# Kernel optimization log

Hardware: AMD Instinct MI355X
Metric: run time of the kernel (lower is better)

The kernel has to match this reference:

```python
import jax, jax.numpy as jnp
import numpy as np
from jax import lax

C = 128; NH = 8; DH = 16      # attn_channels, heads, head_dim
DI = 256; DS = 16; DC = 4     # hmb d_inner=expand*C, d_state, d_conv
KTOP = 128                    # max(min_focus_tokens, int(W*0.5))
CR = 64; CI = 128             # radar / image channels


def _ln(x, g, b, eps=1e-5):
    m = jnp.mean(x, -1, keepdims=True)
    v = jnp.mean((x - m) ** 2, -1, keepdims=True)
    return (x - m) * lax.rsqrt(v + eps) * g + b


def _conv1x1(x, w):
    return jnp.einsum('bchw,oc->bohw', x, w)


def _forward(image_features, radar_features, W_img, W_rad, g_q, b_q, g_kv, b_kv, g2, b2,
             Ws1, bs1, Ws2, bs2, Wqkv, bqkv, Wo, bo, Wf1, bf1, Wf2, bf2, W_delta,
             gamma, gamma_hmb, Wg, bg, Wfuse, bn_g, bn_b, bn_m, bn_v,
             W_hin, conv_dw, b_dw, W_dt, b_dt, W_Bp, W_Cp, A_log, Dp, W_hout):
    B, Cr, H, W = radar_features.shape
    N = B * H
    img_attn = _conv1x1(image_features, W_img)          # [B,C,H,W]
    rad_attn = _conv1x1(radar_features, W_rad)
    img_seq = img_attn.transpose(0, 2, 3, 1).reshape(N, W, C)
    rad_seq = rad_attn.transpose(0, 2, 3, 1).reshape(N, W, C)
    # progressive focus: per-row top-K image tokens
    si = jnp.concatenate([lax.stop_gradient(rad_seq), img_seq], -1)
    h1 = jax.nn.relu(si @ Ws1.T + bs1)
    score = (h1 @ Ws2.T + bs2)[..., 0]                  # [N,W]
    _, idx = lax.top_k(score, KTOP)
    img_kv = jnp.take_along_axis(img_seq, idx[:, :, None], axis=1)  # [N,K,C]
    # cross attention (torch MultiheadAttention, batch_first)
    q = _ln(rad_seq, g_q, b_q)
    kv = _ln(img_kv, g_kv, b_kv)
    Wq, Wk, Wv = Wqkv[:C], Wqkv[C:2 * C], Wqkv[2 * C:]
    bq_, bk_, bv_ = bqkv[:C], bqkv[C:2 * C], bqkv[2 * C:]
    qh = (q @ Wq.T + bq_).reshape(N, W, NH, DH)
    kh = (kv @ Wk.T + bk_).reshape(N, KTOP, NH, DH)
    vh = (kv @ Wv.T + bv_).reshape(N, KTOP, NH, DH)
    att = jax.nn.softmax(jnp.einsum('nqhd,nkhd->nhqk', qh, kh) / (DH ** 0.5), -1)
    ao = jnp.einsum('nhqk,nkhd->nqhd', att, vh).reshape(N, W, C) @ Wo.T + bo
    rad_seq = rad_seq + ao
    rad_seq = rad_seq + (jax.nn.relu(_ln(rad_seq, g2, b2) @ Wf1.T + bf1) @ Wf2.T + bf2)
    rad_bev = rad_seq.reshape(B, H, W, C).transpose(0, 3, 1, 2)
    delta_attn = _conv1x1(rad_bev, W_delta)
    # HMB-lite: bidirectional selective scan along x (per row)
    xz = _conv1x1(jnp.concatenate([rad_bev, img_attn], 1), W_hin)  # [B,2*DI,H,W]
    x, z = xz[:, :DI], xz[:, DI:]
    xr = x.transpose(0, 2, 1, 3).reshape(N, DI, W)
    zr = z.transpose(0, 2, 3, 1).reshape(N, W, DI)
    xp = jnp.pad(xr, ((0, 0), (0, 0), (DC - 1, 0)))     # causal depthwise conv
    xc = lax.conv_general_dilated(xp, conv_dw[:, None, :], (1,), 'VALID',
                                  feature_group_count=DI,
                                  dimension_numbers=('NCH', 'OIH', 'NCH'))
    xs = jax.nn.silu(xc + b_dw[:, None]).transpose(0, 2, 1)        # [N,W,DI]
    dt = jax.nn.softplus(xs @ W_dt.T + b_dt)            # [N,W,DI]
    Bt = xs @ W_Bp.T                                    # [N,W,DS]
    Ct = xs @ W_Cp.T
    A = -jnp.exp(A_log)                                 # [DI,DS]

    def scan(reverse):
        def step(h, inp):
            x_t, dt_t, B_t, C_t = inp
            h = jnp.exp(dt_t[..., None] * A) * h + (dt_t * x_t)[..., None] * B_t[:, None, :]
            return h, jnp.sum(h * C_t[:, None, :], -1)
        h0 = jnp.zeros((N, DI, DS), xs.dtype)
        seq = (xs.transpose(1, 0, 2), dt.transpose(1, 0, 2),
               Bt.transpose(1, 0, 2), Ct.transpose(1, 0, 2))
        _, ys = lax.scan(step, h0, seq, reverse=reverse)
        return ys.transpose(1, 0, 2)

    y = scan(False) + scan(True) + Dp * xs
    y = y * jax.nn.silu(zr)
    hmb = (y @ W_hout.T).reshape(B, H, W, C).transpose(0, 3, 1, 2)
    delta_hmb = _conv1x1(hmb, W_delta)
    # gate + range mask
    gate = jax.nn.sigmoid(_conv1x1(jnp.concatenate([radar_features, image_features], 1), Wg)
                          + bg[None, :, None, None])
    yv = jnp.arange(H, dtype=radar_features.dtype)
    wmask = jnp.clip(1.0 - 0.7 * yv / (H - 1), 0.3, None)
    gate = gate * wmask[None, None, :, None]
    radar_enh = radar_features + gamma * gate * delta_attn + gamma_hmb * gate * delta_hmb
    fuse_in = jnp.concatenate([radar_enh, image_features], 1)
    fo = lax.conv_general_dilated(fuse_in, Wfuse, (1, 1), 'SAME',
                                  dimension_numbers=('NCHW', 'OIHW', 'NCHW'))
    fo = ((fo - bn_m[None, :, None, None]) * lax.rsqrt(bn_v + 1e-5)[None, :, None, None]
          * bn_g[None, :, None, None] + bn_b[None, :, None, None])
    return jax.nn.relu(fo)


def setup_inputs():
    key = jax.random.key(0)
    ks = list(jax.random.split(key, 24))
    def rn(i, shape, s=0.05):
        return jax.random.normal(ks[i], shape, dtype=jnp.float32) * s
    B, H, W = 2, 256, 256
    return dict(
        image_features=jax.random.normal(ks[0], (B, CI, H, W), jnp.float32),
        radar_features=jax.random.normal(ks[1], (B, CR, H, W), jnp.float32),
        W_img=rn(2, (C, CI)), W_rad=rn(3, (C, CR)),
        g_q=jnp.ones(C), b_q=jnp.zeros(C), g_kv=jnp.ones(C), b_kv=jnp.zeros(C),
        g2=jnp.ones(C), b2=jnp.zeros(C),
        Ws1=rn(4, (64, 2 * C)), bs1=jnp.zeros(64), Ws2=rn(5, (1, 64)), bs2=jnp.zeros(1),
        Wqkv=rn(6, (3 * C, C)), bqkv=jnp.zeros(3 * C), Wo=rn(7, (C, C)), bo=jnp.zeros(C),
        Wf1=rn(8, (4 * C, C)), bf1=jnp.zeros(4 * C), Wf2=rn(9, (C, 4 * C)), bf2=jnp.zeros(C),
        W_delta=rn(10, (CR, C)),
        gamma=jnp.array(0.1, jnp.float32), gamma_hmb=jnp.array(0.05, jnp.float32),
        Wg=rn(11, (CR, CR + CI)), bg=jnp.zeros(CR),
        Wfuse=rn(12, (CR + CI, CR + CI, 3, 3)),
        bn_g=jnp.ones(CR + CI), bn_b=jnp.zeros(CR + CI),
        bn_m=jnp.zeros(CR + CI), bn_v=jnp.ones(CR + CI),
        W_hin=rn(13, (2 * DI, 2 * C)), conv_dw=rn(14, (DI, DC)), b_dw=jnp.zeros(DI),
        W_dt=rn(15, (DI, DI)), b_dt=jnp.full((DI,), 0.5, jnp.float32),
        W_Bp=rn(16, (DS, DI)), W_Cp=rn(17, (DS, DI)),
        A_log=jnp.log(jnp.broadcast_to(jnp.arange(1, DS + 1, dtype=jnp.float32), (DI, DS))),
        Dp=jnp.full((DI,), 0.01, jnp.float32),
        W_hout=rn(18, (C, DI)),
    )


def reference(image_features, radar_features, W_img, W_rad, g_q, b_q, g_kv, b_kv, g2, b2,
              Ws1, bs1, Ws2, bs2, Wqkv, bqkv, Wo, bo, Wf1, bf1, Wf2, bf2, W_delta,
              gamma, gamma_hmb, Wg, bg, Wfuse, bn_g, bn_b, bn_m, bn_v,
              W_hin, conv_dw, b_dw, W_dt, b_dt, W_Bp, W_Cp, A_log, Dp, W_hout):
    return _forward(image_features, radar_features, W_img, W_rad, g_q, b_q, g_kv, b_kv, g2, b2,
                    Ws1, bs1, Ws2, bs2, Wqkv, bqkv, Wo, bo, Wf1, bf1, Wf2, bf2, W_delta,
                    gamma, gamma_hmb, Wg, bg, Wfuse, bn_g, bn_b, bn_m, bn_v,
                    W_hin, conv_dw, b_dw, W_dt, b_dt, W_Bp, W_Cp, A_log, Dp, W_hout)
```

## Files before the change

### kernel.cpp

```cpp
#include <hip/hip_runtime.h>
#include <hip/hip_bf16.h>
#include <cstddef>


#define PTOK   131072
#define WSEQ   256
#define HWPIX  65536

typedef unsigned short u16;
typedef unsigned int   u32;
typedef __bf16 bf16x8 __attribute__((ext_vector_type(8)));
typedef float  f32x4  __attribute__((ext_vector_type(4)));

__device__ __forceinline__ float b2f(u16 u) { return __uint_as_float((u32)u << 16); }
__device__ __forceinline__ u16   f2b(float f) {
    u32 x = __float_as_uint(f);
    return (u16)((x + 0x7fffu + ((x >> 16) & 1u)) >> 16);
}
__device__ __forceinline__ u16 f2b_fast(float f) {
    return __builtin_bit_cast(u16, (__bf16)f);
}
__device__ __forceinline__ u32 pk2(float a, float b) {
    return (u32)f2b(a) | ((u32)f2b(b) << 16);
}
__device__ __forceinline__ void unpack8(uint4 p, float* v) {
    const u32 a[4] = {p.x, p.y, p.z, p.w};
#pragma unroll
    for (int q = 0; q < 4; ++q) {
        v[2 * q]     = b2f((u16)(a[q] & 0xffffu));
        v[2 * q + 1] = b2f((u16)(a[q] >> 16));
    }
}
__device__ __forceinline__ void load32(const u16* p, float* v) {
    uint4 a = *(const uint4*)p, b = *(const uint4*)(p + 8);
    uint4 c = *(const uint4*)(p + 16), d = *(const uint4*)(p + 24);
    unpack8(a, v); unpack8(b, v + 8); unpack8(c, v + 16); unpack8(d, v + 24);
}

constexpr int AM_NCHW = 0, AM_TOK = 1, AM_LN = 2, AM_LNG = 3, AM_CAT = 4, AM_FIN = 5;
constexpr int EP_NONE = 0, EP_RELU = 1, EP_RES = 2, EP_SP = 3;

template<int AM, int EPI>
__global__ __launch_bounds__(256)
void mgemm(const void* __restrict__ Apv, const void* __restrict__ Ap2v,
           const void* __restrict__ Ap3v, const void* __restrict__ Ap4v,
           const int* __restrict__ gidx, const float* __restrict__ stats,
           const float* __restrict__ lng, const float* __restrict__ lnb,
           const float* __restrict__ dpv,
           int K, int Cin,
           const float* __restrict__ Bw, const float* __restrict__ Bw2,
           const float* __restrict__ bias,
           u16* __restrict__ Cout, int O, int Ostride)
{
    __shared__ u16 Als[128 * 72];
    __shared__ u16 Bls[128 * 72];
    const int tid = threadIdx.x;
    const int t0 = blockIdx.x * 128;
    const int o0 = blockIdx.y * 128;
    const int lane = tid & 63, wv = tid >> 6;
    const int wm = (wv & 1) * 64, wn = (wv >> 1) * 64;
    const int fc = lane & 15, quad = lane >> 4;

    f32x4 acc[4][4];
#pragma unroll
    for (int i = 0; i < 4; ++i)
#pragma unroll
        for (int j = 0; j < 4; ++j) acc[i][j] = {0.f, 0.f, 0.f, 0.f};

    const int srow = tid >> 1;
    const int sseg = (tid & 1) * 32;

    float mrow = 0.f, rrow = 1.f;
    int grow = t0 + srow;
    if (AM == AM_LN) { mrow = stats[2 * (t0 + srow)]; rrow = stats[2 * (t0 + srow) + 1]; }
    if (AM == AM_LNG) {
        const int ar = t0 + srow;
        grow = (ar >> 7) * 256 + (gidx[ar] & 255);
        mrow = stats[2 * ar]; rrow = stats[2 * ar + 1];
    }

    for (int kc0 = 0; kc0 < K; kc0 += 64) {
        if (AM == AM_NCHW) {
            const float* Af = (const float*)Apv;
            const int tl = tid & 127, cg = (tid >> 7) * 32;
            const int t = t0 + tl;
            const size_t base = (size_t)(t >> 16) * (size_t)Cin * HWPIX + (size_t)(t & (HWPIX - 1));
#pragma unroll 8
            for (int p = 0; p < 32; ++p) {
                const int c = kc0 + cg + p;
                Als[tl * 72 + cg + p] = f2b(Af[base + (size_t)c * HWPIX]);
            }
        } else if (AM == AM_FIN) {
            const int cb = kc0 + sseg;
            const size_t base = (size_t)(t0 + srow) * 256 + cb;
            float vy[32], vb[32], vx[32], vz[32];
            load32((const u16*)Apv  + base, vy);
            load32((const u16*)Ap2v + base, vb);
            load32((const u16*)Ap3v + base, vx);
            load32((const u16*)Ap4v + base, vz);
            float v[32];
#pragma unroll
            for (int p = 0; p < 32; ++p) {
                const float dp = dpv[cb + p];
                const float zz = vz[p];
                const float tot = vy[p] + vb[p] + dp * vx[p];
                v[p] = tot * (zz / (1.f + __expf(-zz)));
            }
            uint4 q0, q1, q2, q3;
            q0.x = pk2(v[0], v[1]);   q0.y = pk2(v[2], v[3]);   q0.z = pk2(v[4], v[5]);   q0.w = pk2(v[6], v[7]);
            q1.x = pk2(v[8], v[9]);   q1.y = pk2(v[10], v[11]); q1.z = pk2(v[12], v[13]); q1.w = pk2(v[14], v[15]);
            q2.x = pk2(v[16], v[17]); q2.y = pk2(v[18], v[19]); q2.z = pk2(v[20], v[21]); q2.w = pk2(v[22], v[23]);
            q3.x = pk2(v[24], v[25]); q3.y = pk2(v[26], v[27]); q3.z = pk2(v[28], v[29]); q3.w = pk2(v[30], v[31]);
            uint4* dst = (uint4*)&Als[srow * 72 + sseg];
            dst[0] = q0; dst[1] = q1; dst[2] = q2; dst[3] = q3;
        } else {
            const u16* src; int rs, cb, row;
            if (AM == AM_CAT) {
                src = (kc0 & 128) ? (const u16*)Ap2v : (const u16*)Apv;
                rs = 128; cb = (kc0 & 127) + sseg; row = t0 + srow;
            } else if (AM == AM_LNG) {
                src = (const u16*)Apv; rs = 128; cb = kc0 + sseg; row = grow;
            } else {
                src = (const u16*)Apv; rs = K; cb = kc0 + sseg; row = t0 + srow;
            }
            const u16* rp = src + (size_t)row * rs + cb;
            uint4 pa = *(const uint4*)rp;
            uint4 pb = *(const uint4*)(rp + 8);
            uint4 pc = *(const uint4*)(rp + 16);
            uint4 pd = *(const uint4*)(rp + 24);
            if (AM == AM_LN || AM == AM_LNG) {
                float v[32];
                unpack8(pa, v); unpack8(pb, v + 8); unpack8(pc, v + 16); unpack8(pd, v + 24);
                const int c0 = cb;
#pragma unroll
                for (int p = 0; p < 32; ++p)
                    v[p] = (v[p] - mrow) * rrow * lng[c0 + p] + lnb[c0 + p];
                uint4 q0, q1, q2, q3;
                q0.x = pk2(v[0], v[1]);   q0.y = pk2(v[2], v[3]);   q0.z = pk2(v[4], v[5]);   q0.w = pk2(v[6], v[7]);
                q1.x = pk2(v[8], v[9]);   q1.y = pk2(v[10], v[11]); q1.z = pk2(v[12], v[13]); q1.w = pk2(v[14], v[15]);
                q2.x = pk2(v[16], v[17]); q2.y = pk2(v[18], v[19]); q2.z = pk2(v[20], v[21]); q2.w = pk2(v[22], v[23]);
                q3.x = pk2(v[24], v[25]); q3.y = pk2(v[26], v[27]); q3.z = pk2(v[28], v[29]); q3.w = pk2(v[30], v[31]);
                pa = q0; pb = q1; pc = q2; pd = q3;
            }
            uint4* dst = (uint4*)&Als[srow * 72 + sseg];
            dst[0] = pa; dst[1] = pb; dst[2] = pc; dst[3] = pd;
        }
        {
            const int og = o0 + srow;
            const bool ok = og < O;
            uint4 q0 = {0,0,0,0}, q1 = {0,0,0,0}, q2 = {0,0,0,0}, q3 = {0,0,0,0};
            if (ok) {
                const float* rp;
                if (Bw2 && og >= 16) rp = Bw2 + (size_t)(og - 16) * K + kc0 + sseg;
                else                 rp = Bw  + (size_t)og * K + kc0 + sseg;
                float v[32];
#pragma unroll
                for (int p = 0; p < 8; ++p) {
                    const float4 f = *(const float4*)(rp + p * 4);
                    v[p * 4 + 0] = f.x; v[p * 4 + 1] = f.y; v[p * 4 + 2] = f.z; v[p * 4 + 3] = f.w;
                }
                q0.x = pk2(v[0], v[1]);   q0.y = pk2(v[2], v[3]);   q0.z = pk2(v[4], v[5]);   q0.w = pk2(v[6], v[7]);
                q1.x = pk2(v[8], v[9]);   q1.y = pk2(v[10], v[11]); q1.z = pk2(v[12], v[13]); q1.w = pk2(v[14], v[15]);
                q2.x = pk2(v[16], v[17]); q2.y = pk2(v[18], v[19]); q2.z = pk2(v[20], v[21]); q2.w = pk2(v[22], v[23]);
                q3.x = pk2(v[24], v[25]); q3.y = pk2(v[26], v[27]); q3.z = pk2(v[28], v[29]); q3.w = pk2(v[30], v[31]);
            }
            uint4* dst = (uint4*)&Bls[srow * 72 + sseg];
            dst[0] = q0; dst[1] = q1; dst[2] = q2; dst[3] = q3;
        }
        __syncthreads();
#pragma unroll
        for (int kc = 0; kc < 64; kc += 32) {
            bf16x8 aF[4], bF[4];
#pragma unroll
            for (int mt = 0; mt < 4; ++mt)
                aF[mt] = *(const bf16x8*)&Als[(wm + mt * 16 + fc) * 72 + kc + quad * 8];
#pragma unroll
            for (int nt = 0; nt < 4; ++nt)
                bF[nt] = *(const bf16x8*)&Bls[(wn + nt * 16 + fc) * 72 + kc + quad * 8];
#pragma unroll
            for (int mt = 0; mt < 4; ++mt)
#pragma unroll
                for (int nt = 0; nt < 4; ++nt)
                    acc[mt][nt] = __builtin_amdgcn_mfma_f32_16x16x32_bf16(aF[mt], bF[nt], acc[mt][nt], 0, 0, 0);
        }
        __syncthreads();
    }

#pragma unroll
    for (int nt = 0; nt < 4; ++nt) {
        const int o = o0 + wn + nt * 16 + fc;
        if (o >= O) continue;
        const float bv = bias ? bias[o] : 0.f;
#pragma unroll
        for (int mt = 0; mt < 4; ++mt) {
#pragma unroll
            for (int reg = 0; reg < 4; ++reg) {
                const int t = t0 + wm + mt * 16 + quad * 4 + reg;
                float v = acc[mt][nt][reg] + bv;
                if (EPI == EP_RELU) v = fmaxf(v, 0.f);
                if (EPI == EP_SP)   v = fmaxf(v, 0.f) + log1pf(expf(-fabsf(v)));
                u16* dst = Cout + (size_t)t * Ostride + o;
                if (EPI == EP_RES)  v += b2f(*dst);
                *dst = f2b(v);
            }
        }
    }
}

__global__ __launch_bounds__(256)
void conv3x3_mfma(const u16* __restrict__ fin, const u16* __restrict__ Wc,
                  const float* __restrict__ bn_g, const float* __restrict__ bn_b,
                  const float* __restrict__ bn_m, const float* __restrict__ bn_v,
                  float* __restrict__ out)
{
    __shared__ u16 Als[128 * 72];
    __shared__ u16 Bls[128 * 72];
    const int tid = threadIdx.x;
    const int t0 = blockIdx.x * 128;
    const int o0 = blockIdx.y * 128;
    const int lane = tid & 63, wv = tid >> 6;
    const int wm = (wv & 1) * 64, wn = (wv >> 1) * 64;
    const int fc = lane & 15, quad = lane >> 4;

    f32x4 acc[4][4];
#pragma unroll
    for (int i = 0; i < 4; ++i)
#pragma unroll
        for (int j = 0; j < 4; ++j) acc[i][j] = {0.f, 0.f, 0.f, 0.f};

    const int srow = tid >> 1;
    const int sseg = (tid & 1) * 32;
    const int t = t0 + srow;
    const int h = (t >> 8) & 255, w = t & 255;

    for (int chunk = 0; chunk < 27; ++chunk) {
        const int kk = chunk / 3;
        const int c0 = (chunk % 3) * 64;
        const int kh = kk / 3, kw = kk % 3;
        {
            const int hh = h + kh - 1, ww = w + kw - 1;
            const bool ok = ((unsigned)hh < 256u) && ((unsigned)ww < 256u);
            uint4 p0 = {0,0,0,0}, p1 = {0,0,0,0}, p2 = {0,0,0,0}, p3 = {0,0,0,0};
            if (ok) {
                const u16* rp = fin + (size_t)(t + (kh - 1) * 256 + (kw - 1)) * 192 + c0 + sseg;
                p0 = *(const uint4*)rp; p1 = *(const uint4*)(rp + 8);
                p2 = *(const uint4*)(rp + 16); p3 = *(const uint4*)(rp + 24);
            }
            uint4* dst = (uint4*)&Als[srow * 72 + sseg];
            dst[0] = p0; dst[1] = p1; dst[2] = p2; dst[3] = p3;
        }
        {
            const int orow = srow;
            const bool ok = (o0 + orow) < 192;
            uint4 p0 = {0,0,0,0}, p1 = {0,0,0,0}, p2 = {0,0,0,0}, p3 = {0,0,0,0};
            if (ok) {
                const u16* rp = Wc + (size_t)kk * 36864 + (size_t)(o0 + orow) * 192 + c0 + sseg;
                p0 = *(const uint4*)rp; p1 = *(const uint4*)(rp + 8);
                p2 = *(const uint4*)(rp + 16); p3 = *(const uint4*)(rp + 24);
            }
            uint4* dst = (uint4*)&Bls[orow * 72 + sseg];
            dst[0] = p0; dst[1] = p1; dst[2] = p2; dst[3] = p3;
        }
        __syncthreads();
#pragma unroll
        for (int kc = 0; kc < 64; kc += 32) {
            bf16x8 aF[4], bF[4];
#pragma unroll
            for (int mt = 0; mt < 4; ++mt)
                aF[mt] = *(const bf16x8*)&Als[(wm + mt * 16 + fc) * 72 + kc + quad * 8];
#pragma unroll
            for (int nt = 0; nt < 4; ++nt)
                bF[nt] = *(const bf16x8*)&Bls[(wn + nt * 16 + fc) * 72 + kc + quad * 8];
#pragma unroll
            for (int mt = 0; mt < 4; ++mt)
#pragma unroll
                for (int nt = 0; nt < 4; ++nt)
                    acc[mt][nt] = __builtin_amdgcn_mfma_f32_16x16x32_bf16(aF[mt], bF[nt], acc[mt][nt], 0, 0, 0);
        }
        __syncthreads();
    }

    const int bb = t0 >> 16, hb = (t0 >> 8) & 255, w0 = t0 & 255;
#pragma unroll
    for (int nt = 0; nt < 4; ++nt) {
        const int o = o0 + wn + nt * 16 + fc;
        if (o >= 192) continue;
        const float sc = bn_g[o] * rsqrtf(bn_v[o] + 1e-5f);
        const float sh = bn_b[o] - bn_m[o] * sc;
        float* op = out + (size_t)(bb * 192 + o) * HWPIX + (size_t)hb * 256;
#pragma unroll
        for (int mt = 0; mt < 4; ++mt) {
#pragma unroll
            for (int reg = 0; reg < 4; ++reg) {
                const int wq = w0 + wm + mt * 16 + quad * 4 + reg;
                op[wq] = fmaxf(acc[mt][nt][reg] * sc + sh, 0.f);
            }
        }
    }
}

__global__ __launch_bounds__(256)
void stats_kernel(const u16* __restrict__ X, float* __restrict__ MR, int ntok)
{
    const int r = blockIdx.x * 4 + (threadIdx.x >> 6);
    const int lane = threadIdx.x & 63;
    if (r >= ntok) return;
    const u16* row = X + (size_t)r * 128;
    const float x0 = b2f(row[lane]), x1 = b2f(row[lane + 64]);
    float s = x0 + x1;
#pragma unroll
    for (int off = 32; off; off >>= 1) s += __shfl_xor(s, off);
    const float m = s * (1.f / 128.f);
    const float e0 = x0 - m, e1 = x1 - m;
    float v = e0 * e0 + e1 * e1;
#pragma unroll
    for (int off = 32; off; off >>= 1) v += __shfl_xor(v, off);
    if (lane == 0) { MR[2 * r] = m; MR[2 * r + 1] = rsqrtf(v * (1.f / 128.f) + 1e-5f); }
}

__global__ __launch_bounds__(256)
void kv_stats_kernel(const u16* __restrict__ I, const int* __restrict__ idx,
                     float* __restrict__ MRKV)
{
    const int r = blockIdx.x * 4 + (threadIdx.x >> 6);
    const int lane = threadIdx.x & 63;
    if (r >= 65536) return;
    const int n = r >> 7;
    const int w = idx[r] & 255;
    const u16* row = I + (size_t)(n * 256 + w) * 128;
    const float x0 = b2f(row[lane]), x1 = b2f(row[lane + 64]);
    float s = x0 + x1;
#pragma unroll
    for (int off = 32; off; off >>= 1) s += __shfl_xor(s, off);
    const float m = s * (1.f / 128.f);
    const float e0 = x0 - m, e1 = x1 - m;
    float v = e0 * e0 + e1 * e1;
#pragma unroll
    for (int off = 32; off; off >>= 1) v += __shfl_xor(v, off);
    if (lane == 0) { MRKV[2 * r] = m; MRKV[2 * r + 1] = rsqrtf(v * (1.f / 128.f) + 1e-5f); }
}

__global__ __launch_bounds__(256)
void score_select_kernel(const u16* __restrict__ radS, const u16* __restrict__ imgS,
                         const float* __restrict__ Ws1, const float* __restrict__ bs1,
                         const float* __restrict__ Ws2, const float* __restrict__ bs2,
                         int* __restrict__ idx)
{
    __shared__ float WT[256][64];
    const int tid = threadIdx.x, n = blockIdx.x;
    for (int i = tid; i < 16384; i += 256) { const int j = i >> 8, c = i & 255; WT[c][j] = Ws1[i]; }
    __syncthreads();
    float acc[64];
#pragma unroll
    for (int j = 0; j < 64; ++j) acc[j] = 0.f;
    const int t = n * WSEQ + tid;
    const u16* r0 = radS + (size_t)t * 128;
    const u16* r1 = imgS + (size_t)t * 128;
    for (int c = 0; c < 128; ++c) {
        const float v = b2f(r0[c]);
#pragma unroll
        for (int j = 0; j < 64; ++j) acc[j] += v * WT[c][j];
    }
    for (int c = 0; c < 128; ++c) {
        const float v = b2f(r1[c]);
#pragma unroll
        for (int j = 0; j < 64; ++j) acc[j] += v * WT[128 + c][j];
    }
    float s = bs2[0];
#pragma unroll
    for (int j = 0; j < 64; ++j) s += fmaxf(acc[j] + bs1[j], 0.f) * Ws2[j];
    __syncthreads();
    float* sc = &WT[0][0];
    sc[tid] = s;
    __syncthreads();
    int rank = 0;
    for (int j = 0; j < 256; ++j) {
        const float sj = sc[j];
        rank += (sj > s) || (sj == s && j < tid);
    }
    if (rank < 128) idx[n * 128 + rank] = tid;
}

__global__ __launch_bounds__(128, 2)
void attn_mfma_kernel(u16* __restrict__ qh, const u16* __restrict__ khvh)
{
    __shared__ u16 Pls[128 * 136];
    __shared__ u16 Vt[16 * 136];
    const int tid  = threadIdx.x;
    const int n    = blockIdx.x >> 1;
    const int half = blockIdx.x & 1;
    const int h    = blockIdx.y;
    const int lane = tid & 63, wv = tid >> 6;
    const int fc = lane & 15, quad = lane >> 4;
    const int wq0 = half * 128 + wv * 64;
    const int pq0 = wv * 64;

    const size_t qrow0 = (size_t)(n * 256 + wq0) * 128 + h * 16;
    const size_t krow0 = (size_t)(n * 128) * 256 + h * 16;

    {
        const int k = tid;
        const u16* src = khvh + krow0 + (size_t)k * 256 + 128;
        const uint4 a = *(const uint4*)src;
        const uint4 b = *(const uint4*)(src + 8);
        const u32 wA[4] = {a.x, a.y, a.z, a.w};
        const u32 wB[4] = {b.x, b.y, b.z, b.w};
#pragma unroll
        for (int p = 0; p < 4; ++p) {
            Vt[(2 * p)     * 136 + k] = (u16)(wA[p] & 0xffffu);
            Vt[(2 * p + 1) * 136 + k] = (u16)(wA[p] >> 16);
            Vt[(8 + 2 * p)     * 136 + k] = (u16)(wB[p] & 0xffffu);
            Vt[(8 + 2 * p + 1) * 136 + k] = (u16)(wB[p] >> 16);
        }
    }

    const uint4 z4 = {0u, 0u, 0u, 0u};
    uint4 qf[4], kf[8];
#pragma unroll
    for (int mt = 0; mt < 4; ++mt)
        qf[mt] = (quad < 2)
            ? *(const uint4*)(qh + qrow0 + (size_t)(mt * 16 + fc) * 128 + quad * 8)
            : z4;
#pragma unroll
    for (int nt = 0; nt < 8; ++nt)
        kf[nt] = (quad < 2)
            ? *(const uint4*)(khvh + krow0 + (size_t)(nt * 16 + fc) * 256 + quad * 8)
            : z4;

    f32x4 s[4][8];
#pragma unroll
    for (int mt = 0; mt < 4; ++mt)
#pragma unroll
        for (int nt = 0; nt < 8; ++nt) s[mt][nt] = {0.f, 0.f, 0.f, 0.f};
#pragma unroll
    for (int mt = 0; mt < 4; ++mt)
#pragma unroll
        for (int nt = 0; nt < 8; ++nt)
            s[mt][nt] = __builtin_amdgcn_mfma_f32_16x16x32_bf16(
                __builtin_bit_cast(bf16x8, qf[mt]),
                __builtin_bit_cast(bf16x8, kf[nt]), s[mt][nt], 0, 0, 0);

    const float cl2 = 0.25f * 1.44269504088896f;
#pragma unroll
    for (int mt = 0; mt < 4; ++mt) {
#pragma unroll
        for (int reg = 0; reg < 4; ++reg) {
            float m = s[mt][0][reg];
#pragma unroll
            for (int nt = 1; nt < 8; ++nt) m = fmaxf(m, s[mt][nt][reg]);
#pragma unroll
            for (int off = 1; off < 16; off <<= 1) m = fmaxf(m, __shfl_xor(m, off));
            const float nmc = -m * cl2;
            float l = 0.f;
#pragma unroll
            for (int nt = 0; nt < 8; ++nt) {
                const float p = exp2f(fmaf(s[mt][nt][reg], cl2, nmc));
                s[mt][nt][reg] = p;
                l += p;
            }
#pragma unroll
            for (int off = 1; off < 16; off <<= 1) l += __shfl_xor(l, off);
            const float iv = 1.f / l;
            const int prow = (pq0 + mt * 16 + quad * 4 + reg) * 136;
#pragma unroll
            for (int nt = 0; nt < 8; ++nt)
                Pls[prow + nt * 16 + fc] = f2b_fast(s[mt][nt][reg] * iv);
        }
    }

    __syncthreads();

    f32x4 o[4];
#pragma unroll
    for (int mt = 0; mt < 4; ++mt) o[mt] = {0.f, 0.f, 0.f, 0.f};
#pragma unroll
    for (int ks = 0; ks < 4; ++ks) {
        const bf16x8 vb = *(const bf16x8*)&Vt[fc * 136 + ks * 32 + quad * 8];
#pragma unroll
        for (int mt = 0; mt < 4; ++mt) {
            const bf16x8 pa = *(const bf16x8*)&Pls[(pq0 + mt * 16 + fc) * 136 + ks * 32 + quad * 8];
            o[mt] = __builtin_amdgcn_mfma_f32_16x16x32_bf16(pa, vb, o[mt], 0, 0, 0);
        }
    }

#pragma unroll
    for (int mt = 0; mt < 4; ++mt) {
#pragma unroll
        for (int reg = 0; reg < 4; ++reg) {
            qh[qrow0 + (size_t)(mt * 16 + quad * 4 + reg) * 128 + fc] = f2b_fast(o[mt][reg]);
        }
    }
}

__global__ __launch_bounds__(256)
void dwconv_kernel(u16* __restrict__ x, const float* __restrict__ kw,
                   const float* __restrict__ bdw)
{
    const int di = threadIdx.x;
    const int n = blockIdx.x;
    const float k0 = kw[di * 4 + 0], k1 = kw[di * 4 + 1];
    const float k2 = kw[di * 4 + 2], k3 = kw[di * 4 + 3];
    const float bb = bdw[di];
    float x3 = 0.f, x2 = 0.f, x1 = 0.f;
    for (int w = 0; w < 256; ++w) {
        const size_t o = (size_t)(n * WSEQ + w) * 256 + di;
        const float x0 = b2f(x[o]);
        const float v = x3 * k0 + x2 * k1 + x1 * k2 + x0 * k3 + bb;
        x[o] = f2b(v * (1.f / (1.f + __expf(-v))));
        x3 = x2; x2 = x1; x1 = x0;
    }
}

__global__ __launch_bounds__(256)
void scan_kernel(const u16* __restrict__ xs, const u16* __restrict__ dt,
                 const u16* __restrict__ btct, const float* __restrict__ A_log,
                 u16* __restrict__ yf, u16* __restrict__ yb)
{
    __shared__ float Bs[256][16];
    __shared__ float Cs[256][16];
    const int di = threadIdx.x;
    const int n = blockIdx.x & 255;
    const int dir = blockIdx.x >> 8;
    for (int i = di; i < 256 * 32; i += 256) {
        const int w = i >> 5, c = i & 31;
        const float v = b2f(btct[(size_t)(n * WSEQ + w) * 32 + c]);
        if (c < 16) Bs[w][c] = v; else Cs[w][c - 16] = v;
    }
    __syncthreads();
    float a[16];
#pragma unroll
    for (int s = 0; s < 16; ++s) a[s] = -__expf(A_log[di * 16 + s]);
    float h[16];
#pragma unroll
    for (int s = 0; s < 16; ++s) h[s] = 0.f;
    u16* yo = dir ? yb : yf;
    for (int i = 0; i < 256; ++i) {
        const int w = dir ? 255 - i : i;
        const size_t t = (size_t)(n * WSEQ + w);
        const float dtv = b2f(dt[t * 256 + di]);
        const float xv = b2f(xs[t * 256 + di]);
        const float dx = dtv * xv;
        float yv = 0.f;
#pragma unroll
        for (int s = 0; s < 16; ++s) {
            const float e = __expf(dtv * a[s]);
            h[s] = e * h[s] + dx * Bs[w][s];
            yv += h[s] * Cs[w][s];
        }
        yo[t * 256 + di] = f2b(yv);
    }
}

__global__ __launch_bounds__(256)
void precomb_kernel(const u16* __restrict__ rad3, u16* __restrict__ hmb,
                    const float* __restrict__ gamma, const float* __restrict__ gammah)
{
    const size_t i = (size_t)blockIdx.x * 256 + threadIdx.x;
    hmb[i] = f2b(gamma[0] * b2f(rad3[i]) + gammah[0] * b2f(hmb[i]));
}

__global__ __launch_bounds__(256)
void gate_kernel(const float* __restrict__ radar, const float* __restrict__ image,
                 const float* __restrict__ Wg, const float* __restrict__ bg,
                 const u16* __restrict__ dcomb, u16* __restrict__ fin)
{
    __shared__ float WT[192][64];
    const int tid = threadIdx.x;
    const int bh = blockIdx.x;
    const int b = bh >> 8, h = bh & 255;
    for (int i = tid; i < 64 * 192; i += 256) { const int o = i / 192, c = i % 192; WT[c][o] = Wg[i]; }
    __syncthreads();
    float acc[64];
#pragma unroll
    for (int o = 0; o < 64; ++o) acc[o] = 0.f;
    const size_t rbase = (size_t)b * 64 * HWPIX + (size_t)h * 256 + tid;
    const size_t ibase = (size_t)b * 128 * HWPIX + (size_t)h * 256 + tid;
    for (int c = 0; c < 64; ++c) {
        const float v = radar[rbase + (size_t)c * HWPIX];
#pragma unroll
        for (int o = 0; o < 64; ++o) acc[o] += v * WT[c][o];
    }
    for (int c = 0; c < 128; ++c) {
        const float v = image[ibase + (size_t)c * HWPIX];
#pragma unroll
        for (int o = 0; o < 64; ++o) acc[o] += v * WT[64 + c][o];
    }
    const float wm = fmaxf(1.f - 0.7f * (float)h * (1.f / 255.f), 0.3f);
    const size_t t = (size_t)bh * 256 + tid;
    u16* fo = fin + t * 192;
    for (int o = 0; o < 64; ++o) {
        const float gate = wm / (1.f + __expf(-(acc[o] + bg[o])));
        fo[o] = f2b(radar[rbase + (size_t)o * HWPIX] + gate * b2f(dcomb[t * 64 + o]));
    }
    for (int c = 0; c < 128; ++c)
        fo[64 + c] = f2b(image[ibase + (size_t)c * HWPIX]);
}

__global__ __launch_bounds__(256)
void wprep_kernel(const float* __restrict__ Wfuse, u16* __restrict__ Wc)
{
    const int i = blockIdx.x * 256 + threadIdx.x;
    if (i >= 9 * 192 * 192) return;
    const int kk = i / 36864, r = i % 36864;
    const int o = r / 192, c = r % 192;
    Wc[i] = f2b(Wfuse[o * 1728 + c * 9 + kk]);
}

extern "C" void kernel_launch(void* const* d_in, const int* in_sizes, int n_in,
                              void* d_out, int out_size, void* d_ws, size_t ws_size,
                              hipStream_t stream)
{
    const float* image  = (const float*)d_in[0];
    const float* radar  = (const float*)d_in[1];
    const float* W_img  = (const float*)d_in[2];
    const float* W_rad  = (const float*)d_in[3];
    const float* g_q    = (const float*)d_in[4];
    const float* b_q    = (const float*)d_in[5];
    const float* g_kv   = (const float*)d_in[6];
    const float* b_kv   = (const float*)d_in[7];
    const float* g2     = (const float*)d_in[8];
    const float* b2     = (const float*)d_in[9];
    const float* Ws1    = (const float*)d_in[10];
    const float* bs1    = (const float*)d_in[11];
    const float* Ws2    = (const float*)d_in[12];
    const float* bs2    = (const float*)d_in[13];
    const float* Wqkv   = (const float*)d_in[14];
    const float* bqkv   = (const float*)d_in[15];
    const float* Wo     = (const float*)d_in[16];
    const float* bo     = (const float*)d_in[17];
    const float* Wf1    = (const float*)d_in[18];
    const float* bf1    = (const float*)d_in[19];
    const float* Wf2    = (const float*)d_in[20];
    const float* bf2    = (const float*)d_in[21];
    const float* W_delta= (const float*)d_in[22];
    const float* gamma  = (const float*)d_in[23];
    const float* gammah = (const float*)d_in[24];
    const float* Wg     = (const float*)d_in[25];
    const float* bg     = (const float*)d_in[26];
    const float* Wfuse  = (const float*)d_in[27];
    const float* bn_g   = (const float*)d_in[28];
    const float* bn_b   = (const float*)d_in[29];
    const float* bn_m   = (const float*)d_in[30];
    const float* bn_v   = (const float*)d_in[31];
    const float* W_hin  = (const float*)d_in[32];
    const float* conv_dw= (const float*)d_in[33];
    const float* b_dw   = (const float*)d_in[34];
    const float* W_dt   = (const float*)d_in[35];
    const float* b_dt   = (const float*)d_in[36];
    const float* W_Bp   = (const float*)d_in[37];
    const float* W_Cp   = (const float*)d_in[38];
    const float* A_log  = (const float*)d_in[39];
    const float* Dp     = (const float*)d_in[40];
    const float* W_hout = (const float*)d_in[41];
    float* out = (float*)d_out;

    u16* wsu = (u16*)d_ws;
    u16* R = wsu;
    u16* I = wsu + 16777216u;
    u16* U = wsu + 33554432u;
    u16* V = wsu + 67108864u;
    u16* Wc = wsu + 100663296u;
    float* ftail = (float*)(wsu + 100995072u);
    float* MR    = ftail;
    float* MRKV  = ftail + 262144u;
    int*   IDX   = (int*)(ftail + 393216u);

    u16* ob  = (u16*)d_out;
    u16* QH  = ob;
    u16* KVH = ob + 16777216u;
    u16* T1  = ob;
    u16* DT  = ob;
    u16* BC  = ob + 16777216u;
    u16* YF  = ob + 18874368u;
    u16* HMB = ob + 35651584u;
    u16* YB  = I;
    u16* DC  = V;

    wprep_kernel<<<1296, 256, 0, stream>>>(Wfuse, Wc);

    mgemm<AM_NCHW, EP_NONE><<<dim3(1024, 1), 256, 0, stream>>>(image, nullptr, nullptr, nullptr, nullptr, nullptr, nullptr, nullptr, nullptr, 128, 128, W_img, nullptr, nullptr, I, 128, 128);
    mgemm<AM_NCHW, EP_NONE><<<dim3(1024, 1), 256, 0, stream>>>(radar, nullptr, nullptr, nullptr, nullptr, nullptr, nullptr, nullptr, nullptr,  64,  64, W_rad, nullptr, nullptr, R, 128, 128);

    score_select_kernel<<<512, 256, 0, stream>>>(R, I, Ws1, bs1, Ws2, bs2, IDX);

    stats_kernel<<<32768, 256, 0, stream>>>(R, MR, PTOK);
    kv_stats_kernel<<<16384, 256, 0, stream>>>(I, IDX, MRKV);

    mgemm<AM_LN,  EP_NONE><<<dim3(1024, 1), 256, 0, stream>>>(R, nullptr, nullptr, nullptr, nullptr, MR, g_q, b_q, nullptr, 128, 0, Wqkv, nullptr, bqkv, QH, 128, 128);
    mgemm<AM_LNG, EP_NONE><<<dim3(512, 2), 256, 0, stream>>>(I, nullptr, nullptr, nullptr, IDX, MRKV, g_kv, b_kv, nullptr, 128, 0, Wqkv + 16384, nullptr, bqkv + 128, KVH, 256, 256);

    attn_mfma_kernel<<<dim3(1024, 8), 128, 0, stream>>>(QH, KVH);
    mgemm<AM_TOK, EP_RES><<<dim3(1024, 1), 256, 0, stream>>>(QH, nullptr, nullptr, nullptr, nullptr, nullptr, nullptr, nullptr, nullptr, 128, 0, Wo, nullptr, bo, R, 128, 128);

    stats_kernel<<<32768, 256, 0, stream>>>(R, MR, PTOK);
    for (int hfl = 0; hfl < 2; ++hfl) {
        const size_t off = (size_t)hfl * 65536u;
        mgemm<AM_LN,  EP_RELU><<<dim3(512, 4), 256, 0, stream>>>(R + off * 128, nullptr, nullptr, nullptr, nullptr, MR + off * 2, g2, b2, nullptr, 128, 0, Wf1, nullptr, bf1, T1, 512, 512);
        mgemm<AM_TOK, EP_RES ><<<dim3(512, 1), 256, 0, stream>>>(T1, nullptr, nullptr, nullptr, nullptr, nullptr, nullptr, nullptr, nullptr, 512, 0, Wf2, nullptr, bf2, R + off * 128, 128, 128);
    }

    mgemm<AM_CAT, EP_NONE><<<dim3(1024, 2), 256, 0, stream>>>(R, I, nullptr, nullptr, nullptr, nullptr, nullptr, nullptr, nullptr, 256, 0, W_hin, nullptr, nullptr, U, 256, 256);
    mgemm<AM_CAT, EP_NONE><<<dim3(1024, 2), 256, 0, stream>>>(R, I, nullptr, nullptr, nullptr, nullptr, nullptr, nullptr, nullptr, 256, 0, W_hin + 65536, nullptr, nullptr, V, 256, 256);

    dwconv_kernel<<<512, 256, 0, stream>>>(U, conv_dw, b_dw);

    for (int hfl = 0; hfl < 2; ++hfl) {
        const size_t off = (size_t)hfl * 65536u;
        u16* xs = U + off * 256;
        u16* z  = V + off * 256;
        mgemm<AM_TOK, EP_SP  ><<<dim3(512, 2), 256, 0, stream>>>(xs, nullptr, nullptr, nullptr, nullptr, nullptr, nullptr, nullptr, nullptr, 256, 0, W_dt, nullptr, b_dt, DT, 256, 256);
        mgemm<AM_TOK, EP_NONE><<<dim3(512, 1), 256, 0, stream>>>(xs, nullptr, nullptr, nullptr, nullptr, nullptr, nullptr, nullptr, nullptr, 256, 0, W_Bp, W_Cp, nullptr, BC, 32, 32);
        scan_kernel<<<512, 256, 0, stream>>>(xs, DT, BC, A_log, YF, YB);
        mgemm<AM_FIN, EP_NONE><<<dim3(512, 1), 256, 0, stream>>>(YF, YB, xs, z, nullptr, nullptr, nullptr, nullptr, Dp, 256, 0, W_hout, nullptr, nullptr, HMB, 128, 128);
        precomb_kernel<<<32768, 256, 0, stream>>>(R + off * 128, HMB, gamma, gammah);
        mgemm<AM_TOK, EP_NONE><<<dim3(512, 1), 256, 0, stream>>>(HMB, nullptr, nullptr, nullptr, nullptr, nullptr, nullptr, nullptr, nullptr, 128, 0, W_delta, nullptr, nullptr, DC + off * 64, 64, 64);
    }

    gate_kernel<<<512, 256, 0, stream>>>(radar, image, Wg, bg, DC, U);

    conv3x3_mfma<<<dim3(1024, 2), 256, 0, stream>>>(U, Wc, bn_g, bn_b, bn_m, bn_v, out);
}
```

Baseline: 1.916 ms.

## Restructure 3x3 conv to cover all 192 output channels and reuse halo row

The conv3x3 kernel now has each block compute all 192 output channels, each wave taking 96 columns, instead of splitting the outputs across two blocks with half the second tile padded. This removes the wasted MFMA work on the padding and the duplicated input loads. It loads one 130-row input strip per kernel row and channel chunk and reuses it for all three kw taps by shifting the shared-memory row offset, so the input is read about three times less often. The block index is swizzled to change the order in which tiles are scheduled. In exchange the kernel uses more accumulator registers (24 tiles), more LDS and launches half as many blocks, which may lower occupancy.

```diff
diff --git a/kernel.cpp b/kernel.cpp
--- a/kernel.cpp
+++ b/kernel.cpp
@@ -213,81 +213,88 @@
                   const float* __restrict__ bn_m, const float* __restrict__ bn_v,
                   float* __restrict__ out)
 {
-    __shared__ u16 Als[128 * 72];
-    __shared__ u16 Bls[128 * 72];
+    __shared__ u16 Als[130 * 72];
+    __shared__ u16 Bls[192 * 72];
     const int tid = threadIdx.x;
-    const int t0 = blockIdx.x * 128;
-    const int o0 = blockIdx.y * 128;
+    const int bid = ((int)blockIdx.x & 7) * 128 + ((int)blockIdx.x >> 3);
+    const int t0 = bid * 128;
     const int lane = tid & 63, wv = tid >> 6;
-    const int wm = (wv & 1) * 64, wn = (wv >> 1) * 64;
+    const int wm = (wv & 1) * 64, wn = (wv >> 1) * 96;
     const int fc = lane & 15, quad = lane >> 4;
-
-    f32x4 acc[4][4];
+    const int b = t0 >> 16, h = (t0 >> 8) & 255, w0 = t0 & 255;
+
+    f32x4 acc[4][6];
 #pragma unroll
     for (int i = 0; i < 4; ++i)
 #pragma unroll
-        for (int j = 0; j < 4; ++j) acc[i][j] = {0.f, 0.f, 0.f, 0.f};
-
-    const int srow = tid >> 1;
-    const int sseg = (tid & 1) * 32;
-    const int t = t0 + srow;
-    const int h = (t >> 8) & 255, w = t & 255;
-
-    for (int chunk = 0; chunk < 27; ++chunk) {
-        const int kk = chunk / 3;
-        const int c0 = (chunk % 3) * 64;
-        const int kh = kk / 3, kw = kk % 3;
-        {
-            const int hh = h + kh - 1, ww = w + kw - 1;
-            const bool ok = ((unsigned)hh < 256u) && ((unsigned)ww < 256u);
-            uint4 p0 = {0,0,0,0}, p1 = {0,0,0,0}, p2 = {0,0,0,0}, p3 = {0,0,0,0};
-            if (ok) {
-                const u16* rp = fin + (size_t)(t + (kh - 1) * 256 + (kw - 1)) * 192 + c0 + sseg;
-                p0 = *(const uint4*)rp; p1 = *(const uint4*)(rp + 8);
-                p2 = *(const uint4*)(rp + 16); p3 = *(const uint4*)(rp + 24);
-            }
-            uint4* dst = (uint4*)&Als[srow * 72 + sseg];
-            dst[0] = p0; dst[1] = p1; dst[2] = p2; dst[3] = p3;
-        }
-        {
-            const int orow = srow;
-            const bool ok = (o0 + orow) < 192;
-            uint4 p0 = {0,0,0,0}, p1 = {0,0,0,0}, p2 = {0,0,0,0}, p3 = {0,0,0,0};
-            if (ok) {
-                const u16* rp = Wc + (size_t)kk * 36864 + (size_t)(o0 + orow) * 192 + c0 + sseg;
-                p0 = *(const uint4*)rp; p1 = *(const uint4*)(rp + 8);
-                p2 = *(const uint4*)(rp + 16); p3 = *(const uint4*)(rp + 24);
-            }
-            uint4* dst = (uint4*)&Bls[orow * 72 + sseg];
-            dst[0] = p0; dst[1] = p1; dst[2] = p2; dst[3] = p3;
-        }
-        __syncthreads();
-#pragma unroll
-        for (int kc = 0; kc < 64; kc += 32) {
-            bf16x8 aF[4], bF[4];
-#pragma unroll
-            for (int mt = 0; mt < 4; ++mt)
-                aF[mt] = *(const bf16x8*)&Als[(wm + mt * 16 + fc) * 72 + kc + quad * 8];
-#pragma unroll
-            for (int nt = 0; nt < 4; ++nt)
-                bF[nt] = *(const bf16x8*)&Bls[(wn + nt * 16 + fc) * 72 + kc + quad * 8];
-#pragma unroll
-            for (int mt = 0; mt < 4; ++mt)
-#pragma unroll
-                for (int nt = 0; nt < 4; ++nt)
-                    acc[mt][nt] = __builtin_amdgcn_mfma_f32_16x16x32_bf16(aF[mt], bF[nt], acc[mt][nt], 0, 0, 0);
-        }
-        __syncthreads();
-    }
-
-    const int bb = t0 >> 16, hb = (t0 >> 8) & 255, w0 = t0 & 255;
-#pragma unroll
-    for (int nt = 0; nt < 4; ++nt) {
-        const int o = o0 + wn + nt * 16 + fc;
-        if (o >= 192) continue;
+        for (int j = 0; j < 6; ++j) acc[i][j] = {0.f, 0.f, 0.f, 0.f};
+
+    for (int kh = 0; kh < 3; ++kh) {
+        const int hh = h + kh - 1;
+        const bool okh = (unsigned)hh < 256u;
+        const size_t rowbase = (size_t)((b * 256 + hh) * 256) * 192;
+        for (int cc = 0; cc < 3; ++cc) {
+            const int c0 = cc * 64;
+            __syncthreads();
+#pragma unroll
+            for (int it = 0; it < 2; ++it) {
+                const int task = tid + it * 256;
+                if (task < 260) {
+                    const int r = task >> 1, seg = (task & 1) * 32;
+                    const int w = w0 + r - 1;
+                    uint4 p0 = {0,0,0,0}, p1 = {0,0,0,0}, p2 = {0,0,0,0}, p3 = {0,0,0,0};
+                    if (okh && (unsigned)w < 256u) {
+                        const u16* rp = fin + rowbase + (size_t)w * 192 + c0 + seg;
+                        p0 = *(const uint4*)rp;        p1 = *(const uint4*)(rp + 8);
+                        p2 = *(const uint4*)(rp + 16); p3 = *(const uint4*)(rp + 24);
+                    }
+                    uint4* dst = (uint4*)&Als[r * 72 + seg];
+                    dst[0] = p0; dst[1] = p1; dst[2] = p2; dst[3] = p3;
+                }
+            }
+            for (int kw = 0; kw < 3; ++kw) {
+                if (kw) __syncthreads();
+                {
+                    const int kk = kh * 3 + kw;
+                    const int r0 = tid >> 1, s0 = (tid & 1) * 32;
+                    const u16* rp = Wc + (size_t)kk * 36864 + (size_t)r0 * 192 + c0 + s0;
+                    uint4* dst = (uint4*)&Bls[r0 * 72 + s0];
+                    dst[0] = *(const uint4*)rp;        dst[1] = *(const uint4*)(rp + 8);
+                    dst[2] = *(const uint4*)(rp + 16); dst[3] = *(const uint4*)(rp + 24);
+                    if (tid < 128) {
+                        const int r1 = 128 + r0, s1 = s0;
+                        const u16* rq = Wc + (size_t)kk * 36864 + (size_t)r1 * 192 + c0 + s1;
+                        uint4* dst2 = (uint4*)&Bls[r1 * 72 + s1];
+                        dst2[0] = *(const uint4*)rq;        dst2[1] = *(const uint4*)(rq + 8);
+                        dst2[2] = *(const uint4*)(rq + 16); dst2[3] = *(const uint4*)(rq + 24);
+                    }
+                }
+                __syncthreads();
+#pragma unroll
+                for (int kc = 0; kc < 64; kc += 32) {
+                    bf16x8 aF[4], bF[6];
+#pragma unroll
+                    for (int mt = 0; mt < 4; ++mt)
+                        aF[mt] = *(const bf16x8*)&Als[(kw + wm + mt * 16 + fc) * 72 + kc + quad * 8];
+#pragma unroll
+                    for (int nt = 0; nt < 6; ++nt)
+                        bF[nt] = *(const bf16x8*)&Bls[(wn + nt * 16 + fc) * 72 + kc + quad * 8];
+#pragma unroll
+                    for (int mt = 0; mt < 4; ++mt)
+#pragma unroll
+                        for (int nt = 0; nt < 6; ++nt)
+                            acc[mt][nt] = __builtin_amdgcn_mfma_f32_16x16x32_bf16(aF[mt], bF[nt], acc[mt][nt], 0, 0, 0);
+                }
+            }
+        }
+    }
+
+#pragma unroll
+    for (int nt = 0; nt < 6; ++nt) {
+        const int o = wn + nt * 16 + fc;
         const float sc = bn_g[o] * rsqrtf(bn_v[o] + 1e-5f);
         const float sh = bn_b[o] - bn_m[o] * sc;
-        float* op = out + (size_t)(bb * 192 + o) * HWPIX + (size_t)hb * 256;
+        float* op = out + (size_t)(b * 192 + o) * HWPIX + (size_t)h * 256;
 #pragma unroll
         for (int mt = 0; mt < 4; ++mt) {
 #pragma unroll
@@ -718,5 +725,5 @@
 
     gate_kernel<<<512, 256, 0, stream>>>(radar, image, Wg, bg, DC, U);
 
-    conv3x3_mfma<<<dim3(1024, 2), 256, 0, stream>>>(U, Wc, bn_g, bn_b, bn_m, bn_v, out);
-}
+    conv3x3_mfma<<<dim3(1024), 256, 0, stream>>>(U, Wc, bn_g, bn_b, bn_m, bn_v, out);
+}
```

Result: slower. 1.963 ms (+2.4%).
